# Optimization experiments

Measured on AMD Instinct MI355X. Metric: run time of the kernel, lower is better.

Reference implementation:

```python
import jax, jax.numpy as jnp
import numpy as np

B, T, C, H = 8, 1024, 768, 12
HD = C // H  # 64

def setup_inputs() -> dict:
    key = jax.random.key(0)
    ks = jax.random.split(key, 5)
    s = 0.02
    return {
        "x": jax.random.normal(ks[0], (B, T, C), dtype=jnp.float32),
        "w_attn": jax.random.normal(ks[1], (C, 3 * C), dtype=jnp.float32) * s,
        "b_attn": jnp.zeros((3 * C,), dtype=jnp.float32),
        "w_proj": jax.random.normal(ks[2], (C, C), dtype=jnp.float32) * s,
        "b_proj": jnp.zeros((C,), dtype=jnp.float32),
    }

def reference(x, w_attn, b_attn, w_proj, b_proj):
    Bx, Tx, Cx = x.shape
    qkv = x @ w_attn + b_attn                      # [B,T,3C]
    q, k, v = jnp.split(qkv, 3, axis=-1)
    # [B,H,T,hd]
    q = q.reshape(Bx, Tx, H, HD).transpose(0, 2, 1, 3)
    k = k.reshape(Bx, Tx, H, HD).transpose(0, 2, 1, 3)
    v = v.reshape(Bx, Tx, H, HD).transpose(0, 2, 1, 3)
    scale = 1.0 / jnp.sqrt(jnp.asarray(HD, dtype=x.dtype))
    scores = jnp.einsum('bhqd,bhkd->bhqk', q, k) * scale  # [B,H,T,T]
    causal = jnp.tril(jnp.ones((Tx, Tx), dtype=bool))
    scores = jnp.where(causal, scores, jnp.asarray(-jnp.inf, dtype=x.dtype))
    weights = jax.nn.softmax(scores, axis=-1)
    y = jnp.einsum('bhqk,bhkd->bhqd', weights, v)  # [B,H,T,hd]
    y = y.transpose(0, 2, 1, 3).reshape(Bx, Tx, Cx)
    return y @ w_proj + b_proj
```

## Files before the change

kernel.cpp:

```cpp
#include <hip/hip_runtime.h>
#include <cstdint>
#include <cstddef>

#define B_  8
#define T_  1024
#define C_  768
#define H_  12
#define HD_ 64
#define K3_ 2304

typedef unsigned short u16;
typedef __attribute__((ext_vector_type(8))) short bf16x8;
typedef __attribute__((ext_vector_type(4))) float f32x4;

#define MFMA __builtin_amdgcn_mfma_f32_16x16x32_bf16

__device__ __forceinline__ u16 f2bf(float f) {
    unsigned u = __builtin_bit_cast(unsigned, f);
    u += 0x7fffu + ((u >> 16) & 1u);
    return (u16)(u >> 16);
}

__device__ __forceinline__ unsigned pk2bf(float a, float b) {
    unsigned ua = __builtin_bit_cast(unsigned, a) + 0x8000u;
    unsigned ub = __builtin_bit_cast(unsigned, b) + 0x8000u;
    return (ua >> 16) | (ub & 0xffff0000u);
}

#define GLL16(gp, lp) __builtin_amdgcn_global_load_lds( \
    (__attribute__((address_space(1))) unsigned int*)(gp), \
    (__attribute__((address_space(3))) unsigned int*)(lp), 16, 0, 0)

__device__ __forceinline__ void tcvt_tile(const float* __restrict__ in, u16* __restrict__ out,
                                          int R, int Cc, int bx, int by, int tid, float* tile ) {
    int bc = bx * 32, br = by * 32;
    int tx = tid & 31, ty = tid >> 5;
    #pragma unroll
    for (int kk = 0; kk < 32; kk += 8)
        tile[(ty + kk) * 33 + tx] = in[(size_t)(br + ty + kk) * Cc + bc + tx];
    __syncthreads();
    #pragma unroll
    for (int kk = 0; kk < 32; kk += 8)
        out[(size_t)(bc + ty + kk) * R + br + tx] = f2bf(tile[tx * 33 + ty + kk]);
}

__global__ void prep(const float* __restrict__ x, u16* __restrict__ xb,
                     const float* __restrict__ wa, u16* __restrict__ wat,
                     const float* __restrict__ wp, u16* __restrict__ wpt) {
    __shared__ float tile[32 * 33];
    int bid = blockIdx.x, tid = threadIdx.x;
    if (bid < 6144) {
        int i = bid * 256 + tid;
        float4 v = ((const float4*)x)[i];
        ushort4 o;
        o.x = f2bf(v.x); o.y = f2bf(v.y); o.z = f2bf(v.z); o.w = f2bf(v.w);
        ((ushort4*)xb)[i] = o;
    } else if (bid < 6144 + 1728) {
        int b = bid - 6144;
        tcvt_tile(wa, wat, C_, K3_, b % 72, b / 72, tid, tile);
    } else {
        int b = bid - 7872;
        tcvt_tile(wp, wpt, C_, C_, b % 24, b / 24, tid, tile);
    }
}

__launch_bounds__(256)
__global__ void gemm_qkv(const u16* __restrict__ A, const u16* __restrict__ Bt,
                         const float* __restrict__ bias,
                         u16* __restrict__ q, u16* __restrict__ k, u16* __restrict__ v) {
    const int K = C_;
    __shared__ __align__(16) u16 SM[16896];
    u16 (*As)[64] = (u16(*)[64])SM;
    u16 (*Bs)[64] = (u16(*)[64])(SM + 8192);
    u16 (*Cs)[132] = (u16(*)[132])SM;
    int tid = threadIdx.x;
    int id = blockIdx.x;
    int xcd = id & 7, jj = id >> 3;
    int m0 = (xcd * 8 + (jj & 7)) * 128;
    int n0 = (jj >> 3) * 128;
    int lane = tid & 63, wv = tid >> 6;
    int wm = (wv >> 1) * 64, wn = (wv & 1) * 64;
    int r16 = lane & 15, quad = lane >> 4;

    f32x4 acc[4][4] = {};
    int srow = tid >> 3;
    int gblk = (tid & 7) ^ (srow & 7);
    const u16* Ag = A  + (size_t)(m0 + srow) * K + gblk * 8;
    const u16* Bg = Bt + (size_t)(n0 + srow) * K + gblk * 8;
    u16* Al = SM + tid * 8;
    u16* Bl = SM + 8192 + tid * 8;
    int sw = r16 & 7;

    for (int kt = 0; kt < K; kt += 64) {
        #pragma unroll
        for (int s = 0; s < 4; s++) {
            GLL16(Ag + (size_t)(s * 32) * K + kt, Al + s * 2048);
            GLL16(Bg + (size_t)(s * 32) * K + kt, Bl + s * 2048);
        }
        __syncthreads();
        #pragma unroll
        for (int kk = 0; kk < 2; kk++) {
            bf16x8 af[4], bfr[4];
            #pragma unroll
            for (int i = 0; i < 4; i++) af[i]  = *(const bf16x8*)&As[wm + i * 16 + r16][((kk * 4 + quad) ^ sw) * 8];
            #pragma unroll
            for (int j = 0; j < 4; j++) bfr[j] = *(const bf16x8*)&Bs[wn + j * 16 + r16][((kk * 4 + quad) ^ sw) * 8];
            #pragma unroll
            for (int i = 0; i < 4; i++)
                #pragma unroll
                for (int j = 0; j < 4; j++)
                    acc[i][j] = MFMA(af[i], bfr[j], acc[i][j], 0, 0, 0);
        }
        __syncthreads();
    }

    int sec = n0 / C_;
    int cc0 = n0 - sec * C_;
    int b = m0 >> 10, t0 = m0 & 1023;

    if (sec == 2) {
        #pragma unroll
        for (int i = 0; i < 4; i++) {
            #pragma unroll
            for (int j = 0; j < 4; j++) {
                int cc = cc0 + wn + j * 16 + r16;
                float bv = bias[2 * C_ + cc];
                int h = cc >> 6, hd = cc & 63;
                int t = t0 + wm + i * 16 + quad * 4;
                ushort4 ov;
                ov.x = f2bf(acc[i][j][0] + bv); ov.y = f2bf(acc[i][j][1] + bv);
                ov.z = f2bf(acc[i][j][2] + bv); ov.w = f2bf(acc[i][j][3] + bv);
                *(ushort4*)(v + (((size_t)b * H_ + h) * HD_ + hd) * T_ + t) = ov;
            }
        }
    } else {
        float scale = (sec == 0) ? 0.125f : 1.0f;
        u16* dst = (sec == 0) ? q : k;
        #pragma unroll
        for (int i = 0; i < 4; i++)
            #pragma unroll
            for (int j = 0; j < 4; j++) {
                int col = wn + j * 16 + r16;
                float bv = bias[sec * C_ + cc0 + col];
                #pragma unroll
                for (int r = 0; r < 4; r++)
                    Cs[wm + i * 16 + quad * 4 + r][col] = f2bf((acc[i][j][r] + bv) * scale);
            }
        __syncthreads();
        int h0 = cc0 >> 6;
        int rsel = tid >> 4;
        int hs = (tid >> 3) & 1;
        int c8 = (tid & 7) * 8;
        #pragma unroll
        for (int p = 0; p < 8; p++) {
            int rl = p * 16 + rsel;
            uint4 val = *(const uint4*)&Cs[rl][hs * 64 + c8];
            *(uint4*)(dst + (((size_t)b * H_ + h0 + hs) * T_ + t0 + rl) * HD_ + c8) = val;
        }
    }
}

__launch_bounds__(256)
__global__ void gemm_proj(const u16* __restrict__ A, const u16* __restrict__ Bt,
                          const float* __restrict__ bias, float* __restrict__ out) {
    const int K = C_, N = C_;
    __shared__ __align__(16) u16 SM[16384];
    u16 (*As)[64] = (u16(*)[64])SM;
    u16 (*Bs)[64] = (u16(*)[64])(SM + 8192);
    int tid = threadIdx.x;
    int id = blockIdx.x;
    int xcd = id & 7, jj = id >> 3;
    int m0 = (xcd * 8 + (jj & 7)) * 128;
    int n0 = (jj >> 3) * 128;
    int lane = tid & 63, wv = tid >> 6;
    int wm = (wv >> 1) * 64, wn = (wv & 1) * 64;
    int r16 = lane & 15, quad = lane >> 4;

    f32x4 acc[4][4] = {};
    int srow = tid >> 3;
    int gblk = (tid & 7) ^ (srow & 7);
    const u16* Ag = A  + (size_t)(m0 + srow) * K + gblk * 8;
    const u16* Bg = Bt + (size_t)(n0 + srow) * K + gblk * 8;
    u16* Al = SM + tid * 8;
    u16* Bl = SM + 8192 + tid * 8;
    int sw = r16 & 7;

    for (int kt = 0; kt < K; kt += 64) {
        #pragma unroll
        for (int s = 0; s < 4; s++) {
            GLL16(Ag + (size_t)(s * 32) * K + kt, Al + s * 2048);
            GLL16(Bg + (size_t)(s * 32) * K + kt, Bl + s * 2048);
        }
        __syncthreads();
        #pragma unroll
        for (int kk = 0; kk < 2; kk++) {
            bf16x8 af[4], bfr[4];
            #pragma unroll
            for (int i = 0; i < 4; i++) af[i]  = *(const bf16x8*)&As[wm + i * 16 + r16][((kk * 4 + quad) ^ sw) * 8];
            #pragma unroll
            for (int j = 0; j < 4; j++) bfr[j] = *(const bf16x8*)&Bs[wn + j * 16 + r16][((kk * 4 + quad) ^ sw) * 8];
            #pragma unroll
            for (int i = 0; i < 4; i++)
                #pragma unroll
                for (int j = 0; j < 4; j++)
                    acc[i][j] = MFMA(af[i], bfr[j], acc[i][j], 0, 0, 0);
        }
        __syncthreads();
    }

    #pragma unroll
    for (int i = 0; i < 4; i++) {
        #pragma unroll
        for (int j = 0; j < 4; j++) {
            int gn = n0 + wn + j * 16 + r16;
            float bv = bias[gn];
            #pragma unroll
            for (int r = 0; r < 4; r++) {
                int gm = m0 + wm + i * 16 + quad * 4 + r;
                out[(size_t)gm * N + gn] = acc[i][j][r] + bv;
            }
        }
    }
}

__launch_bounds__(256, 2)
__global__ void attn(const u16* __restrict__ q, const u16* __restrict__ k,
                     const u16* __restrict__ v, u16* __restrict__ y) {
    __shared__ __align__(16) u16 Kb[2][64][64];
    __shared__ __align__(16) u16 Vb[2][64][64];
    __shared__ __align__(16) u16 P[4][2][16][72];
    int tid = threadIdx.x, lane = tid & 63, w = tid >> 6;
    int r16 = lane & 15, quad = lane >> 4;
    int id = blockIdx.x;
    int bh = id % 96;
    int bi = id / 96;
    int b = bh / H_, h = bh - b * H_;
    int x = bi * 4 + w;
    int t_lo = x, t_hi = 63 - x;
    int qb_lo = t_lo * 16, qb_hi = t_hi * 16;
    const u16* qh = q + (size_t)bh * T_ * HD_;
    const u16* kh = k + (size_t)bh * T_ * HD_;
    const u16* vh = v + (size_t)bh * HD_ * T_;

    bf16x8 ql0 = *(const bf16x8*)(qh + (size_t)(qb_lo + r16) * HD_ + quad * 8);
    bf16x8 ql1 = *(const bf16x8*)(qh + (size_t)(qb_lo + r16) * HD_ + 32 + quad * 8);
    bf16x8 qh0 = *(const bf16x8*)(qh + (size_t)(qb_hi + r16) * HD_ + quad * 8);
    bf16x8 qh1 = *(const bf16x8*)(qh + (size_t)(qb_hi + r16) * HD_ + 32 + quad * 8);

    f32x4 oL[4] = {}, oH[4] = {};
    float lL = 0.f, lH = 0.f;
    int qyL = qb_lo + r16, qyH = qb_hi + r16;
    int ilo_last = bi;
    int n64 = __builtin_amdgcn_readfirstlane(16 - bi);

    int srow = lane >> 3;
    int scb  = (lane & 7) ^ srow;
    const u16* kst = kh + (size_t)(w * 16 + srow) * HD_ + scb * 8;
    const u16* vst = vh + (size_t)(w * 16 + srow) * T_ + scb * 8;
    int swz = (r16 & 7);

    {
        #pragma unroll
        for (int s2 = 0; s2 < 2; s2++) {
            GLL16(kst + (size_t)(s2 * 8) * HD_, &Kb[0][w * 16 + s2 * 8][0] + lane * 8);
            GLL16(vst + (size_t)(s2 * 8) * T_,  &Vb[0][w * 16 + s2 * 8][0] + lane * 8);
        }
    }
    __syncthreads();

    for (int it = 0; it < n64; ++it) {
        int kv0 = it * 64;
        int buf = it & 1;
        bool lo_on = (it <= ilo_last);
        if (it + 1 < n64) {
            int kvn = kv0 + 64;
            #pragma unroll
            for (int s2 = 0; s2 < 2; s2++) {
                GLL16(kst + (size_t)(kvn + s2 * 8) * HD_, &Kb[buf ^ 1][w * 16 + s2 * 8][0] + lane * 8);
                GLL16(vst + (size_t)(s2 * 8) * T_ + kvn,  &Vb[buf ^ 1][w * 16 + s2 * 8][0] + lane * 8);
            }
        }
        bf16x8 kf[4][2];
        #pragma unroll
        for (int n = 0; n < 4; n++)
            #pragma unroll
            for (int c = 0; c < 2; c++)
                kf[n][c] = *(const bf16x8*)&Kb[buf][n * 16 + r16][((c * 4 + quad) ^ swz) * 8];
        f32x4 sH[4] = {};
        #pragma unroll
        for (int n = 0; n < 4; n++) {
            sH[n] = MFMA(kf[n][0], qh0, sH[n], 0, 0, 0);
            sH[n] = MFMA(kf[n][1], qh1, sH[n], 0, 0, 0);
        }
        if (it == n64 - 1) {
            #pragma unroll
            for (int n = 0; n < 4; n++)
                #pragma unroll
                for (int r = 0; r < 4; r++)
                    if (kv0 + n * 16 + quad * 4 + r > qyH) sH[n][r] = -1e30f;
        }
        #pragma unroll
        for (int n = 0; n < 4; n++) {
            float p0 = __expf(sH[n][0]);
            float p1 = __expf(sH[n][1]);
            float p2 = __expf(sH[n][2]);
            float p3 = __expf(sH[n][3]);
            lH += (p0 + p1) + (p2 + p3);
            uint2 pd; pd.x = pk2bf(p0, p1); pd.y = pk2bf(p2, p3);
            *(uint2*)&P[w][1][r16][n * 16 + quad * 4] = pd;
        }
        if (lo_on) {
            f32x4 sL[4] = {};
            #pragma unroll
            for (int n = 0; n < 4; n++) {
                sL[n] = MFMA(kf[n][0], ql0, sL[n], 0, 0, 0);
                sL[n] = MFMA(kf[n][1], ql1, sL[n], 0, 0, 0);
            }
            if (it == ilo_last) {
                #pragma unroll
                for (int n = 0; n < 4; n++)
                    #pragma unroll
                    for (int r = 0; r < 4; r++)
                        if (kv0 + n * 16 + quad * 4 + r > qyL) sL[n][r] = -1e30f;
            }
            #pragma unroll
            for (int n = 0; n < 4; n++) {
                float p0 = __expf(sL[n][0]);
                float p1 = __expf(sL[n][1]);
                float p2 = __expf(sL[n][2]);
                float p3 = __expf(sL[n][3]);
                lL += (p0 + p1) + (p2 + p3);
                uint2 pd; pd.x = pk2bf(p0, p1); pd.y = pk2bf(p2, p3);
                *(uint2*)&P[w][0][r16][n * 16 + quad * 4] = pd;
            }
        }
        bf16x8 vf[4][2];
        #pragma unroll
        for (int j = 0; j < 4; j++)
            #pragma unroll
            for (int c = 0; c < 2; c++)
                vf[j][c] = *(const bf16x8*)&Vb[buf][j * 16 + r16][((c * 4 + quad) ^ swz) * 8];
        #pragma unroll
        for (int c = 0; c < 2; c++) {
            bf16x8 pfH = *(const bf16x8*)&P[w][1][r16][c * 32 + quad * 8];
            #pragma unroll
            for (int j = 0; j < 4; j++)
                oH[j] = MFMA(vf[j][c], pfH, oH[j], 0, 0, 0);
        }
        if (lo_on) {
            #pragma unroll
            for (int c = 0; c < 2; c++) {
                bf16x8 pfL = *(const bf16x8*)&P[w][0][r16][c * 32 + quad * 8];
                #pragma unroll
                for (int j = 0; j < 4; j++)
                    oL[j] = MFMA(vf[j][c], pfL, oL[j], 0, 0, 0);
            }
        }
        __syncthreads();
    }

    lH += __shfl_xor(lH, 16, 64);
    lH += __shfl_xor(lH, 32, 64);
    lL += __shfl_xor(lL, 16, 64);
    lL += __shfl_xor(lL, 32, 64);
    float invH = 1.f / lH, invL = 1.f / lL;
    int tqH = qb_hi + r16, tqL = qb_lo + r16;
    #pragma unroll
    for (int j = 0; j < 4; j++) {
        ushort4 ovH, ovL;
        ovH.x = f2bf(oH[j][0] * invH); ovH.y = f2bf(oH[j][1] * invH);
        ovH.z = f2bf(oH[j][2] * invH); ovH.w = f2bf(oH[j][3] * invH);
        ovL.x = f2bf(oL[j][0] * invL); ovL.y = f2bf(oL[j][1] * invL);
        ovL.z = f2bf(oL[j][2] * invL); ovL.w = f2bf(oL[j][3] * invL);
        *(ushort4*)(y + ((size_t)b * T_ + tqH) * C_ + h * 64 + j * 16 + quad * 4) = ovH;
        *(ushort4*)(y + ((size_t)b * T_ + tqL) * C_ + h * 64 + j * 16 + quad * 4) = ovL;
    }
}

extern "C" void kernel_launch(void* const* d_in, const int* in_sizes, int n_in,
                              void* d_out, int out_size, void* d_ws, size_t ws_size,
                              hipStream_t stream) {
    const float* x      = (const float*)d_in[0];
    const float* w_attn = (const float*)d_in[1];
    const float* b_attn = (const float*)d_in[2];
    const float* w_proj = (const float*)d_in[3];
    const float* b_proj = (const float*)d_in[4];
    float* out = (float*)d_out;

    char* ws = (char*)d_ws;
    size_t off = 0;
    auto alloc = [&](size_t bytes) {
        void* p = ws + off;
        off += (bytes + 255) & ~(size_t)255;
        return p;
    };
    const size_t M = (size_t)B_ * T_;
    u16* x_bf = (u16*)alloc(M * C_ * 2);
    u16* wat  = (u16*)alloc((size_t)K3_ * C_ * 2);
    u16* wpt  = (u16*)alloc((size_t)C_ * C_ * 2);
    u16* qb   = (u16*)alloc((size_t)B_ * H_ * T_ * HD_ * 2);
    u16* kb   = (u16*)alloc((size_t)B_ * H_ * T_ * HD_ * 2);
    u16* vb   = (u16*)alloc((size_t)B_ * H_ * T_ * HD_ * 2);
    u16* yb   = (u16*)alloc(M * C_ * 2);

    prep<<<6144 + 1728 + 576, 256, 0, stream>>>(x, x_bf, w_attn, wat, w_proj, wpt);
    gemm_qkv<<<8 * 144, 256, 0, stream>>>(x_bf, wat, b_attn, qb, kb, vb);
    attn<<<8 * 96, 256, 0, stream>>>(qb, kb, vb, yb);
    gemm_proj<<<8 * 48, 256, 0, stream>>>(yb, wpt, b_proj, out);
}
```

Measured before the change: 175.6 us.

## Double-buffer K=32 LDS tiles in QKV and projection GEMMs

Both GEMM main loops now use two LDS buffers holding K=32 slices with a matching XOR swizzle. The async global-to-LDS loads for the next slice are issued before the MFMAs on the current slice, and each iteration has one barrier instead of two. The aim is to hide global load latency behind the matrix math. In exchange, each loop runs twice as many iterations, each with less work, which adds barrier and address overhead per iteration.

```diff
diff --git a/kernel.cpp b/kernel.cpp
--- a/kernel.cpp
+++ b/kernel.cpp
@@ -70,8 +70,6 @@
                          u16* __restrict__ q, u16* __restrict__ k, u16* __restrict__ v) {
     const int K = C_;
     __shared__ __align__(16) u16 SM[16896];
-    u16 (*As)[64] = (u16(*)[64])SM;
-    u16 (*Bs)[64] = (u16(*)[64])(SM + 8192);
     u16 (*Cs)[132] = (u16(*)[132])SM;
     int tid = threadIdx.x;
     int id = blockIdx.x;
@@ -83,34 +81,38 @@
     int r16 = lane & 15, quad = lane >> 4;
 
     f32x4 acc[4][4] = {};
-    int srow = tid >> 3;
-    int gblk = (tid & 7) ^ (srow & 7);
-    const u16* Ag = A  + (size_t)(m0 + srow) * K + gblk * 8;
-    const u16* Bg = Bt + (size_t)(n0 + srow) * K + gblk * 8;
-    u16* Al = SM + tid * 8;
-    u16* Bl = SM + 8192 + tid * 8;
-    int sw = r16 & 7;
-
-    for (int kt = 0; kt < K; kt += 64) {
-        #pragma unroll
-        for (int s = 0; s < 4; s++) {
-            GLL16(Ag + (size_t)(s * 32) * K + kt, Al + s * 2048);
-            GLL16(Bg + (size_t)(s * 32) * K + kt, Bl + s * 2048);
-        }
-        __syncthreads();
-        #pragma unroll
-        for (int kk = 0; kk < 2; kk++) {
-            bf16x8 af[4], bfr[4];
-            #pragma unroll
-            for (int i = 0; i < 4; i++) af[i]  = *(const bf16x8*)&As[wm + i * 16 + r16][((kk * 4 + quad) ^ sw) * 8];
-            #pragma unroll
-            for (int j = 0; j < 4; j++) bfr[j] = *(const bf16x8*)&Bs[wn + j * 16 + r16][((kk * 4 + quad) ^ sw) * 8];
-            #pragma unroll
-            for (int i = 0; i < 4; i++)
-                #pragma unroll
-                for (int j = 0; j < 4; j++)
-                    acc[i][j] = MFMA(af[i], bfr[j], acc[i][j], 0, 0, 0);
-        }
+    int srow = tid >> 2;
+    int g = (tid & 3) ^ ((tid >> 3) & 3);
+    const u16* Ag = A  + (size_t)(m0 + srow) * K + g * 8;
+    const u16* Bg = Bt + (size_t)(n0 + srow) * K + g * 8;
+    int srd = (r16 >> 1) & 3;
+
+    auto stage = [&](int kt, int b) {
+        u16* Ab = SM + b * 4096 + tid * 8;
+        u16* Bb = SM + 8192 + b * 4096 + tid * 8;
+        GLL16(Ag + kt, Ab);
+        GLL16(Ag + (size_t)64 * K + kt, Ab + 2048);
+        GLL16(Bg + kt, Bb);
+        GLL16(Bg + (size_t)64 * K + kt, Bb + 2048);
+    };
+
+    stage(0, 0);
+    __syncthreads();
+    for (int it = 0; it < K / 32; ++it) {
+        int buf = it & 1;
+        if (it + 1 < K / 32) stage((it + 1) * 32, buf ^ 1);
+        bf16x8 af[4], bfr[4];
+        #pragma unroll
+        for (int i = 0; i < 4; i++)
+            af[i]  = *(const bf16x8*)&SM[buf * 4096 + (wm + i * 16 + r16) * 32 + ((quad ^ srd) * 8)];
+        #pragma unroll
+        for (int j = 0; j < 4; j++)
+            bfr[j] = *(const bf16x8*)&SM[8192 + buf * 4096 + (wn + j * 16 + r16) * 32 + ((quad ^ srd) * 8)];
+        #pragma unroll
+        for (int i = 0; i < 4; i++)
+            #pragma unroll
+            for (int j = 0; j < 4; j++)
+                acc[i][j] = MFMA(af[i], bfr[j], acc[i][j], 0, 0, 0);
         __syncthreads();
     }
 
@@ -165,8 +167,6 @@
                           const float* __restrict__ bias, float* __restrict__ out) {
     const int K = C_, N = C_;
     __shared__ __align__(16) u16 SM[16384];
-    u16 (*As)[64] = (u16(*)[64])SM;
-    u16 (*Bs)[64] = (u16(*)[64])(SM + 8192);
     int tid = threadIdx.x;
     int id = blockIdx.x;
     int xcd = id & 7, jj = id >> 3;
@@ -177,34 +177,38 @@
     int r16 = lane & 15, quad = lane >> 4;
 
     f32x4 acc[4][4] = {};
-    int srow = tid >> 3;
-    int gblk = (tid & 7) ^ (srow & 7);
-    const u16* Ag = A  + (size_t)(m0 + srow) * K + gblk * 8;
-    const u16* Bg = Bt + (size_t)(n0 + srow) * K + gblk * 8;
-    u16* Al = SM + tid * 8;
-    u16* Bl = SM + 8192 + tid * 8;
-    int sw = r16 & 7;
-
-    for (int kt = 0; kt < K; kt += 64) {
-        #pragma unroll
-        for (int s = 0; s < 4; s++) {
-            GLL16(Ag + (size_t)(s * 32) * K + kt, Al + s * 2048);
-            GLL16(Bg + (size_t)(s * 32) * K + kt, Bl + s * 2048);
-        }
-        __syncthreads();
-        #pragma unroll
-        for (int kk = 0; kk < 2; kk++) {
-            bf16x8 af[4], bfr[4];
-            #pragma unroll
-            for (int i = 0; i < 4; i++) af[i]  = *(const bf16x8*)&As[wm + i * 16 + r16][((kk * 4 + quad) ^ sw) * 8];
-            #pragma unroll
-            for (int j = 0; j < 4; j++) bfr[j] = *(const bf16x8*)&Bs[wn + j * 16 + r16][((kk * 4 + quad) ^ sw) * 8];
-            #pragma unroll
-            for (int i = 0; i < 4; i++)
-                #pragma unroll
-                for (int j = 0; j < 4; j++)
-                    acc[i][j] = MFMA(af[i], bfr[j], acc[i][j], 0, 0, 0);
-        }
+    int srow = tid >> 2;
+    int g = (tid & 3) ^ ((tid >> 3) & 3);
+    const u16* Ag = A  + (size_t)(m0 + srow) * K + g * 8;
+    const u16* Bg = Bt + (size_t)(n0 + srow) * K + g * 8;
+    int srd = (r16 >> 1) & 3;
+
+    auto stage = [&](int kt, int b) {
+        u16* Ab = SM + b * 4096 + tid * 8;
+        u16* Bb = SM + 8192 + b * 4096 + tid * 8;
+        GLL16(Ag + kt, Ab);
+        GLL16(Ag + (size_t)64 * K + kt, Ab + 2048);
+        GLL16(Bg + kt, Bb);
+        GLL16(Bg + (size_t)64 * K + kt, Bb + 2048);
+    };
+
+    stage(0, 0);
+    __syncthreads();
+    for (int it = 0; it < K / 32; ++it) {
+        int buf = it & 1;
+        if (it + 1 < K / 32) stage((it + 1) * 32, buf ^ 1);
+        bf16x8 af[4], bfr[4];
+        #pragma unroll
+        for (int i = 0; i < 4; i++)
+            af[i]  = *(const bf16x8*)&SM[buf * 4096 + (wm + i * 16 + r16) * 32 + ((quad ^ srd) * 8)];
+        #pragma unroll
+        for (int j = 0; j < 4; j++)
+            bfr[j] = *(const bf16x8*)&SM[8192 + buf * 4096 + (wn + j * 16 + r16) * 32 + ((quad ^ srd) * 8)];
+        #pragma unroll
+        for (int i = 0; i < 4; i++)
+            #pragma unroll
+            for (int j = 0; j < 4; j++)
+                acc[i][j] = MFMA(af[i], bfr[j], acc[i][j], 0, 0, 0);
         __syncthreads();
     }
 
```

New measurement: 182.7 us. 1.04x slower.

## Double-buffer LDS tiles in QKV and projection GEMMs

Applied to the files above, without the earlier changes.

Both GEMM kernels now use two LDS buffers for the A and B tiles. The next K-slice is issued with direct global-to-LDS loads while the current slice is consumed by MFMAs, so memory latency can overlap with compute. LDS per block doubles to 64 KB, which may lower occupancy. The one remaining barrier per iteration must also correctly separate reuse of the buffer being refilled.

```diff
diff --git a/kernel.cpp b/kernel.cpp
--- a/kernel.cpp
+++ b/kernel.cpp
@@ -69,9 +69,7 @@
                          const float* __restrict__ bias,
                          u16* __restrict__ q, u16* __restrict__ k, u16* __restrict__ v) {
     const int K = C_;
-    __shared__ __align__(16) u16 SM[16896];
-    u16 (*As)[64] = (u16(*)[64])SM;
-    u16 (*Bs)[64] = (u16(*)[64])(SM + 8192);
+    __shared__ __align__(16) u16 SM[32768];
     u16 (*Cs)[132] = (u16(*)[132])SM;
     int tid = threadIdx.x;
     int id = blockIdx.x;
@@ -87,24 +85,32 @@
     int gblk = (tid & 7) ^ (srow & 7);
     const u16* Ag = A  + (size_t)(m0 + srow) * K + gblk * 8;
     const u16* Bg = Bt + (size_t)(n0 + srow) * K + gblk * 8;
-    u16* Al = SM + tid * 8;
-    u16* Bl = SM + 8192 + tid * 8;
     int sw = r16 & 7;
 
-    for (int kt = 0; kt < K; kt += 64) {
+    auto stage = [&](int kt, int b) {
+        u16* Ab = SM + b * 8192 + tid * 8;
+        u16* Bb = SM + 16384 + b * 8192 + tid * 8;
         #pragma unroll
         for (int s = 0; s < 4; s++) {
-            GLL16(Ag + (size_t)(s * 32) * K + kt, Al + s * 2048);
-            GLL16(Bg + (size_t)(s * 32) * K + kt, Bl + s * 2048);
-        }
-        __syncthreads();
+            GLL16(Ag + (size_t)(s * 32) * K + kt, Ab + s * 2048);
+            GLL16(Bg + (size_t)(s * 32) * K + kt, Bb + s * 2048);
+        }
+    };
+
+    stage(0, 0);
+    __syncthreads();
+    for (int it = 0; it < K / 64; ++it) {
+        int buf = it & 1;
+        if (it + 1 < K / 64) stage((it + 1) * 64, buf ^ 1);
         #pragma unroll
         for (int kk = 0; kk < 2; kk++) {
             bf16x8 af[4], bfr[4];
             #pragma unroll
-            for (int i = 0; i < 4; i++) af[i]  = *(const bf16x8*)&As[wm + i * 16 + r16][((kk * 4 + quad) ^ sw) * 8];
-            #pragma unroll
-            for (int j = 0; j < 4; j++) bfr[j] = *(const bf16x8*)&Bs[wn + j * 16 + r16][((kk * 4 + quad) ^ sw) * 8];
+            for (int i = 0; i < 4; i++)
+                af[i]  = *(const bf16x8*)&SM[buf * 8192 + (wm + i * 16 + r16) * 64 + ((kk * 4 + quad) ^ sw) * 8];
+            #pragma unroll
+            for (int j = 0; j < 4; j++)
+                bfr[j] = *(const bf16x8*)&SM[16384 + buf * 8192 + (wn + j * 16 + r16) * 64 + ((kk * 4 + quad) ^ sw) * 8];
             #pragma unroll
             for (int i = 0; i < 4; i++)
                 #pragma unroll
@@ -164,9 +170,7 @@
 __global__ void gemm_proj(const u16* __restrict__ A, const u16* __restrict__ Bt,
                           const float* __restrict__ bias, float* __restrict__ out) {
     const int K = C_, N = C_;
-    __shared__ __align__(16) u16 SM[16384];
-    u16 (*As)[64] = (u16(*)[64])SM;
-    u16 (*Bs)[64] = (u16(*)[64])(SM + 8192);
+    __shared__ __align__(16) u16 SM[32768];
     int tid = threadIdx.x;
     int id = blockIdx.x;
     int xcd = id & 7, jj = id >> 3;
@@ -181,24 +185,32 @@
     int gblk = (tid & 7) ^ (srow & 7);
     const u16* Ag = A  + (size_t)(m0 + srow) * K + gblk * 8;
     const u16* Bg = Bt + (size_t)(n0 + srow) * K + gblk * 8;
-    u16* Al = SM + tid * 8;
-    u16* Bl = SM + 8192 + tid * 8;
     int sw = r16 & 7;
 
-    for (int kt = 0; kt < K; kt += 64) {
+    auto stage = [&](int kt, int b) {
+        u16* Ab = SM + b * 8192 + tid * 8;
+        u16* Bb = SM + 16384 + b * 8192 + tid * 8;
         #pragma unroll
         for (int s = 0; s < 4; s++) {
-            GLL16(Ag + (size_t)(s * 32) * K + kt, Al + s * 2048);
-            GLL16(Bg + (size_t)(s * 32) * K + kt, Bl + s * 2048);
-        }
-        __syncthreads();
+            GLL16(Ag + (size_t)(s * 32) * K + kt, Ab + s * 2048);
+            GLL16(Bg + (size_t)(s * 32) * K + kt, Bb + s * 2048);
+        }
+    };
+
+    stage(0, 0);
+    __syncthreads();
+    for (int it = 0; it < K / 64; ++it) {
+        int buf = it & 1;
+        if (it + 1 < K / 64) stage((it + 1) * 64, buf ^ 1);
         #pragma unroll
         for (int kk = 0; kk < 2; kk++) {
             bf16x8 af[4], bfr[4];
             #pragma unroll
-            for (int i = 0; i < 4; i++) af[i]  = *(const bf16x8*)&As[wm + i * 16 + r16][((kk * 4 + quad) ^ sw) * 8];
-            #pragma unroll
-            for (int j = 0; j < 4; j++) bfr[j] = *(const bf16x8*)&Bs[wn + j * 16 + r16][((kk * 4 + quad) ^ sw) * 8];
+            for (int i = 0; i < 4; i++)
+                af[i]  = *(const bf16x8*)&SM[buf * 8192 + (wm + i * 16 + r16) * 64 + ((kk * 4 + quad) ^ sw) * 8];
+            #pragma unroll
+            for (int j = 0; j < 4; j++)
+                bfr[j] = *(const bf16x8*)&SM[16384 + buf * 8192 + (wn + j * 16 + r16) * 64 + ((kk * 4 + quad) ^ sw) * 8];
             #pragma unroll
             for (int i = 0; i < 4; i++)
                 #pragma unroll
```

Result: no change. 176.4 us (+0.5%).
